# Performance work log

Hardware: AMD Instinct MI355X
Metric: run time of the kernel (lower is better)

## Reference

```python
import jax, jax.numpy as jnp
import numpy as np

L, N, E, H = 1024, 8, 512, 8


def setup_inputs() -> dict:
    key = jax.random.key(0)
    k1, k2, k3, k4 = jax.random.split(key, 4)
    query = jax.random.normal(k1, (L, N, E), dtype=jnp.float32)
    time = jax.random.normal(k2, (L, N, 1), dtype=jnp.float32) * 1000.0  # timestamps
    in_proj_weight = jax.random.normal(k3, (3 * E, E), dtype=jnp.float32) * 0.02
    in_proj_bias = jnp.zeros((3 * E,), dtype=jnp.float32)
    out_proj_weight = jax.random.normal(k4, (E, E), dtype=jnp.float32) * 0.02
    out_proj_bias = jnp.zeros((E,), dtype=jnp.float32)
    return {
        "query": query,
        "time": time,
        "in_proj_weight": in_proj_weight,
        "in_proj_bias": in_proj_bias,
        "out_proj_weight": out_proj_weight,
        "out_proj_bias": out_proj_bias,
    }


def _temporal_mha(query, time, in_proj_weight, in_proj_bias, out_proj_weight, out_proj_bias):
    # Self-attention path of temporal_multi_head_attention_forward (query is key is value).
    tgt_len, bsz, embed_dim = query.shape
    num_heads = H
    head_dim = embed_dim // num_heads
    scaling = float(head_dim) ** -0.5

    # Temporal bias: tt = time.permute(1,0,2) -> (N, L, 1); alpha[b,i,j] = exp((t_bi - t_bj)/1e6)
    tt = jnp.transpose(time, (1, 0, 2))  # (N, L, 1)
    alpha_time = jnp.exp((tt - jnp.reshape(tt, (bsz, 1, tgt_len))) / 1.0e6)  # (N, L, L)

    # Fused in-projection then chunk into q, k, v.
    qkv = query @ in_proj_weight.T + in_proj_bias  # (L, N, 3E)
    q, k, v = jnp.split(qkv, 3, axis=-1)
    q = q * scaling

    def heads(x):  # (L, N, E) -> (N, H, L, hd)
        return jnp.transpose(x.reshape(tgt_len, bsz, num_heads, head_dim), (1, 2, 0, 3))

    q, k, v = heads(q), heads(k), heads(v)

    # Scores with temporal bias injected (broadcast over heads) -- this is the
    # materialized (N, H, L, L) tensor that breaks the SDPA fusion path.
    scores = jnp.einsum("bhld,bhsd->bhls", q, k) * alpha_time[:, None, :, :]
    attn = jax.nn.softmax(scores, axis=-1)  # dropout_p = 0.0 (inference/reference)

    out = jnp.einsum("bhls,bhsd->bhld", attn, v)  # (N, H, L, hd)
    out = jnp.transpose(out, (2, 0, 1, 3)).reshape(tgt_len, bsz, embed_dim)  # (L, N, E)
    return out @ out_proj_weight.T + out_proj_bias


def reference(query, time, in_proj_weight, in_proj_bias, out_proj_weight, out_proj_bias):
    return _temporal_mha(query, time, in_proj_weight, in_proj_bias, out_proj_weight, out_proj_bias)
```

## Files before the change

kernel.cpp:

```cpp
#include <hip/hip_runtime.h>
#include <cstdint>
#include <cstddef>

typedef unsigned short u16;
typedef unsigned int u32;
typedef __attribute__((ext_vector_type(8))) short short8;
typedef __attribute__((ext_vector_type(4))) float f32x4;
typedef __attribute__((ext_vector_type(16))) float f32x16;

#define L_SEQ 1024
#define N_B   8
#define E_DIM 512
#define H_H   8
#define D_H   64
#define M_ROWS 8192

#if __has_builtin(__builtin_amdgcn_exp2f)
#define EXP2(x) __builtin_amdgcn_exp2f(x)
#else
#define EXP2(x) exp2f(x)
#endif

__device__ __forceinline__ u16 f2bf(float f) {
    u32 u = __float_as_uint(f);
    u32 r = (u + 0x7fffu + ((u >> 16) & 1u)) >> 16;
    return (u16)r;
}

__device__ __forceinline__ u32 cvtpk(float lo, float hi_) {
    u32 r;
    asm("v_cvt_pk_bf16_f32 %0, %1, %2" : "=v"(r) : "v"(lo), "v"(hi_));
    return r;
}

__device__ __forceinline__ void gload16(const void* g, void* l) {
    __builtin_amdgcn_global_load_lds(
        (__attribute__((address_space(1))) void*)(g),
        (__attribute__((address_space(3))) void*)(l), 16, 0, 0);
}

__device__ __forceinline__ short8 ldsw(const u16* base, int row, int c) {
    return *reinterpret_cast<const short8*>(
        reinterpret_cast<const char*>(base) + row * 128 + ((c ^ (row & 7)) << 4));
}

__global__ __launch_bounds__(256) void convert_kernel(
    const float* __restrict__ a, const float* __restrict__ b, const float* __restrict__ c,
    u16* __restrict__ ab, u16* __restrict__ bb, u16* __restrict__ cb)
{
    const int NA = M_ROWS * E_DIM / 4;
    const int NB = 1536 * E_DIM / 4;
    const int i4 = blockIdx.x * 256 + threadIdx.x;
    const float* src; u16* dst; int j;
    if (i4 < NA)           { src = a; dst = ab; j = i4; }
    else if (i4 < NA + NB) { src = b; dst = bb; j = i4 - NA; }
    else                   { src = c; dst = cb; j = i4 - NA - NB; }
    const float4 v = reinterpret_cast<const float4*>(src)[j];
    ushort4 o;
    o.x = f2bf(v.x); o.y = f2bf(v.y); o.z = f2bf(v.z); o.w = f2bf(v.w);
    reinterpret_cast<ushort4*>(dst)[j] = o;
}

template <int MODE, int MI>
__global__ __launch_bounds__(256, 2) void gemm_kernel(
    const u16* __restrict__ A, const u16* __restrict__ B,
    const float* __restrict__ bias, const float* __restrict__ tptr,
    u16* __restrict__ qh, u16* __restrict__ kh, u16* __restrict__ vh,
    float* __restrict__ outf)
{
    constexpr int BM = MI * 32;
    __shared__ __align__(16) u16 Asm_[BM * 64];
    __shared__ __align__(16) u16 Bsm[128 * 64];
    const int tid = threadIdx.x;
    const int lane = tid & 63, w = tid >> 6;
    const int wm = w >> 1, wn = w & 1;
    const int m0 = blockIdx.x * BM, n0 = blockIdx.y * 128;

    f32x4 acc[MI][4];
    #pragma unroll
    for (int mi = 0; mi < MI; ++mi)
        #pragma unroll
        for (int ni = 0; ni < 4; ++ni)
            #pragma unroll
            for (int r = 0; r < 4; ++r) acc[mi][ni][r] = 0.f;

    const int srow = (w << 3) + (lane >> 3);
    const int csrc = ((lane & 7) ^ (lane >> 3)) << 3;

    for (int kt = 0; kt < 8; ++kt) {
        __syncthreads();
        #pragma unroll
        for (int i = 0; i < MI; ++i) {
            const int row = (i << 5) + srow;
            gload16(A + (size_t)(m0 + row) * 512 + (kt << 6) + csrc,
                    (char*)Asm_ + (i << 12) + (w << 10));
        }
        #pragma unroll
        for (int i = 0; i < 4; ++i) {
            const int row = (i << 5) + srow;
            gload16(B + (size_t)(n0 + row) * 512 + (kt << 6) + csrc,
                    (char*)Bsm + (i << 12) + (w << 10));
        }
        __syncthreads();
        #pragma unroll
        for (int k01 = 0; k01 < 2; ++k01) {
            short8 af[MI], bfr[4];
            #pragma unroll
            for (int x = 0; x < MI; ++x)
                af[x] = ldsw(Asm_, wm * (MI * 16) + (x << 4) + (lane & 15),
                             (k01 << 2) + (lane >> 4));
            #pragma unroll
            for (int x = 0; x < 4; ++x)
                bfr[x] = ldsw(Bsm, (wn << 6) + (x << 4) + (lane & 15),
                              (k01 << 2) + (lane >> 4));
            __builtin_amdgcn_s_setprio(1);
            #pragma unroll
            for (int mi = 0; mi < MI; ++mi)
                #pragma unroll
                for (int ni = 0; ni < 4; ++ni)
                    acc[mi][ni] = __builtin_amdgcn_mfma_f32_16x16x32_bf16(
                        af[mi], bfr[ni], acc[mi][ni], 0, 0, 0);
            __builtin_amdgcn_s_setprio(0);
        }
    }

    const int nb = n0 + (wn << 6) + (lane & 15);
    const int mb = m0 + wm * (MI * 16) + ((lane >> 4) << 2);
    float bsv[4];
    #pragma unroll
    for (int ni = 0; ni < 4; ++ni) bsv[ni] = bias[nb + (ni << 4)];
    const int sec = n0 >> 9;

    #pragma unroll
    for (int mi = 0; mi < MI; ++mi) {
        #pragma unroll
        for (int r = 0; r < 4; ++r) {
            const int m = mb + (mi << 4) + r;
            float scale = 1.f;
            if (MODE == 0) {
                if (sec == 0)      scale = 0.18033688f * __expf(tptr[m] * 1e-6f);
                else if (sec == 1) scale = __expf(tptr[m] * -1e-6f);
            }
            #pragma unroll
            for (int ni = 0; ni < 4; ++ni) {
                const int n = nb + (ni << 4);
                const float v = acc[mi][ni][r] + bsv[ni];
                if (MODE == 0) {
                    const int l_seq = m >> 3, bb2 = m & 7;
                    const int hh = (n & 511) >> 6, dd = n & 63;
                    u16* dst = (sec == 0) ? qh : (sec == 1) ? kh : vh;
                    dst[(((size_t)(bb2 << 3) + hh) * L_SEQ + l_seq) * D_H + dd] = f2bf(v * scale);
                } else {
                    outf[(size_t)m * 512 + n] = v;
                }
            }
        }
    }
}

__global__ __launch_bounds__(256) void transpose_v(
    const u16* __restrict__ vh, u16* __restrict__ vt)
{
    __shared__ __align__(16) u16 T[64 * 64];
    const int bh = blockIdx.x, kt = blockIdx.y;
    const u16* src = vh + ((size_t)bh * L_SEQ + kt * 64) * D_H;

    #pragma unroll
    for (int rnd = 0; rnd < 2; ++rnd) {
        const int slot = rnd * 256 + threadIdx.x;
        const int row = slot >> 3, c = slot & 7;
        const uint4 v = *reinterpret_cast<const uint4*>(src + row * 64 + c * 8);
        const int cs = c ^ (row & 7) ^ ((row >> 3) & 7);
        *reinterpret_cast<uint4*>(&T[row * 64 + cs * 8]) = v;
    }
    __syncthreads();
    #pragma unroll
    for (int rnd = 0; rnd < 2; ++rnd) {
        const int slot = rnd * 256 + threadIdx.x;
        const int d = slot >> 3, kc = slot & 7;
        u16 tmp[8];
        #pragma unroll
        for (int j = 0; j < 8; ++j) {
            const int row = kc * 8 + j;
            const int col = (((d >> 3) ^ (row & 7) ^ ((row >> 3) & 7)) << 3) + (d & 7);
            tmp[j] = T[row * 64 + col];
        }
        *reinterpret_cast<uint4*>(vt + ((size_t)bh * D_H + d) * L_SEQ + kt * 64 + kc * 8) =
            *reinterpret_cast<uint4*>(tmp);
    }
}

__global__ __launch_bounds__(128) void attn_kernel(
    const u16* __restrict__ qh, const u16* __restrict__ kh,
    const u16* __restrict__ vt, u16* __restrict__ ao)
{
    __shared__ __align__(16) u16 SM[16384];

    const int tid = threadIdx.x;
    const int lane = tid & 63, w = tid >> 6;
    const int hi = lane >> 5, q31 = lane & 31;
    const int bh = blockIdx.x, qt = blockIdx.y;
    const int b = bh >> 3, h = bh & 7;

    const u16* qrow = qh + ((size_t)bh * L_SEQ + qt * 64 + w * 32 + q31) * D_H;
    short8 qf[4];
    #pragma unroll
    for (int ks = 0; ks < 4; ++ks)
        qf[ks] = *reinterpret_cast<const short8*>(qrow + ks * 16 + hi * 8);

    f32x16 oacc[2];
    #pragma unroll
    for (int d = 0; d < 2; ++d)
        #pragma unroll
        for (int r = 0; r < 16; ++r) oacc[d][r] = 0.f;
    float m_run = -1e30f, l_run = 0.f;

    const u16* kbase = kh + (size_t)bh * L_SEQ * D_H;
    const u16* vbase = vt + (size_t)bh * D_H * L_SEQ;
    const int r8 = lane >> 3;
    const int csrc = ((lane & 7) ^ r8) << 3;

    auto stage = [&](int buf, int kt) {
        #pragma unroll
        for (int i = 0; i < 4; ++i) {
            const int row = (w << 5) + (i << 3) + r8;
            gload16(kbase + (size_t)(kt * 64 + row) * 64 + csrc,
                    (char*)SM + buf * 8192 + (w << 12) + (i << 10));
            gload16(vbase + (size_t)row * 1024 + kt * 64 + csrc,
                    (char*)SM + 16384 + buf * 8192 + (w << 12) + (i << 10));
        }
    };

    int cur = 0;
    stage(0, 0);
    __syncthreads();

    for (int kt = 0; kt < 16; ++kt) {
        if (kt < 15) stage(cur ^ 1, kt + 1);
        const u16* Kc = SM + cur * 4096;
        const u16* Vc = SM + 8192 + cur * 4096;

        f32x16 s[2];
        #pragma unroll
        for (int d = 0; d < 2; ++d)
            #pragma unroll
            for (int r = 0; r < 16; ++r) s[d][r] = 0.f;
        __builtin_amdgcn_s_setprio(1);
        #pragma unroll
        for (int ks = 0; ks < 4; ++ks) {
            const int c = 2 * ks + hi;
            const short8 ka0 = ldsw(Kc, q31, c);
            const short8 ka1 = ldsw(Kc, 32 + q31, c);
            s[0] = __builtin_amdgcn_mfma_f32_32x32x16_bf16(ka0, qf[ks], s[0], 0, 0, 0);
            s[1] = __builtin_amdgcn_mfma_f32_32x32x16_bf16(ka1, qf[ks], s[1], 0, 0, 0);
        }
        __builtin_amdgcn_s_setprio(0);

        float pmax = -1e30f;
        #pragma unroll
        for (int hh = 0; hh < 2; ++hh)
            #pragma unroll
            for (int r = 0; r < 16; ++r) pmax = fmaxf(pmax, s[hh][r]);
        pmax = fmaxf(pmax, __shfl_xor(pmax, 32));
        if (!__all(pmax - m_run <= 8.0f)) {
            const float mn = fmaxf(m_run, pmax);
            const float fr = EXP2(m_run - mn);
            l_run *= fr;
            oacc[0] *= fr; oacc[1] *= fr;
            m_run = mn;
        }
        float p[2][16];
        float sum = 0.f;
        #pragma unroll
        for (int hh = 0; hh < 2; ++hh)
            #pragma unroll
            for (int r = 0; r < 16; ++r) {
                const float e = EXP2(s[hh][r] - m_run);
                p[hh][r] = e; sum += e;
            }
        sum += __shfl_xor(sum, 32);
        l_run += sum;

        __builtin_amdgcn_s_setprio(1);
        #pragma unroll
        for (int ks = 0; ks < 4; ++ks) {
            const int e = ks & 1, hh = ks >> 1;
            const u32 pkA = cvtpk(p[hh][8 * e + 0], p[hh][8 * e + 1]);
            const u32 pkB = cvtpk(p[hh][8 * e + 2], p[hh][8 * e + 3]);
            const u32 pkC = cvtpk(p[hh][8 * e + 4], p[hh][8 * e + 5]);
            const u32 pkD = cvtpk(p[hh][8 * e + 6], p[hh][8 * e + 7]);
            const u32 keep0 = hi ? pkC : pkA, keep1 = hi ? pkD : pkB;
            const u32 send0 = hi ? pkA : pkC, send1 = hi ? pkB : pkD;
            const u32 r0 = (u32)__shfl_xor((int)send0, 32);
            const u32 r1 = (u32)__shfl_xor((int)send1, 32);
            union { u32 u[4]; short8 v; } pf;
            pf.u[0] = hi ? r0 : keep0;  pf.u[1] = hi ? r1 : keep1;
            pf.u[2] = hi ? keep0 : r0;  pf.u[3] = hi ? keep1 : r1;
            const int c = 2 * ks + hi;
            const short8 va0 = ldsw(Vc, q31, c);
            const short8 va1 = ldsw(Vc, 32 + q31, c);
            oacc[0] = __builtin_amdgcn_mfma_f32_32x32x16_bf16(va0, pf.v, oacc[0], 0, 0, 0);
            oacc[1] = __builtin_amdgcn_mfma_f32_32x32x16_bf16(va1, pf.v, oacc[1], 0, 0, 0);
        }
        __builtin_amdgcn_s_setprio(0);
        __syncthreads();
        cur ^= 1;
    }

    const float inv = 1.f / l_run;
    float* myO = (float*)SM + w * 2080;
    #pragma unroll
    for (int dh = 0; dh < 2; ++dh)
        #pragma unroll
        for (int r = 0; r < 16; ++r) {
            const int d = dh * 32 + (r & 3) + 8 * (r >> 2) + 4 * hi;
            myO[q31 * 65 + d] = oacc[dh][r] * inv;
        }
    __syncthreads();
    #pragma unroll
    for (int i = 0; i < 4; ++i) {
        const int slot = i * 64 + lane;
        const int qq = slot >> 3, dc = slot & 7;
        u16 outv[8];
        #pragma unroll
        for (int j = 0; j < 8; ++j) outv[j] = f2bf(myO[qq * 65 + dc * 8 + j]);
        const int lrow = qt * 64 + w * 32 + qq;
        *reinterpret_cast<uint4*>(ao + ((size_t)lrow * N_B + b) * E_DIM + h * 64 + dc * 8) =
            *reinterpret_cast<uint4*>(outv);
    }
}

extern "C" void kernel_launch(void* const* d_in, const int* in_sizes, int n_in,
                              void* d_out, int out_size, void* d_ws, size_t ws_size,
                              hipStream_t stream) {
    const float* query = (const float*)d_in[0];
    const float* timep = (const float*)d_in[1];
    const float* w_in  = (const float*)d_in[2];
    const float* b_in  = (const float*)d_in[3];
    const float* w_out = (const float*)d_in[4];
    const float* b_out = (const float*)d_in[5];
    float* out = (float*)d_out;

    u16* ws = (u16*)d_ws;
    const size_t SZ = (size_t)M_ROWS * E_DIM;
    u16* Abf  = ws;
    u16* Wibf = Abf + SZ;
    u16* Wobf = Wibf + 1536 * 512;
    u16* qhb  = Wobf + 512 * 512;
    u16* khb  = qhb + SZ;
    u16* vhb  = khb + SZ;
    u16* vtb  = vhb + SZ;
    u16* aob  = vtb + SZ;

    convert_kernel<<<5120, 256, 0, stream>>>(query, w_in, w_out, Abf, Wibf, Wobf);
    gemm_kernel<0, 4><<<dim3(64, 12), 256, 0, stream>>>(
        Abf, Wibf, b_in, timep, qhb, khb, vhb, nullptr);
    transpose_v<<<dim3(64, 16), 256, 0, stream>>>(vhb, vtb);
    attn_kernel<<<dim3(64, 16), 128, 0, stream>>>(qhb, khb, vtb, aob);
    gemm_kernel<1, 2><<<dim3(128, 4), 256, 0, stream>>>(
        aob, Wobf, b_out, nullptr, nullptr, nullptr, nullptr, out);
}
```

Baseline: 142.7 us.

## Load K/V fragments directly from global into registers in single-wave attention blocks

The attention kernel drops the LDS double-buffered K/V staging and block-level barriers. Each 64-thread block (one wave, 32 query rows) now reads its MFMA operand fragments for K and V straight from global memory into registers. The grid is flattened to 2048 blocks with a swizzled block-to-(head, q-tile) mapping so that blocks sharing a head are likely to hit the same cache. This removes LDS traffic and syncs, but each wave now fetches K/V on its own with no explicit prefetch, which doubles global/L2 reads and exposes load latency.

```diff
diff --git a/kernel.cpp b/kernel.cpp
--- a/kernel.cpp
+++ b/kernel.cpp
@@ -190,19 +190,20 @@
     }
 }
 
-__global__ __launch_bounds__(128) void attn_kernel(
+__global__ __launch_bounds__(64) void attn_kernel(
     const u16* __restrict__ qh, const u16* __restrict__ kh,
     const u16* __restrict__ vt, u16* __restrict__ ao)
 {
-    __shared__ __align__(16) u16 SM[16384];
-
-    const int tid = threadIdx.x;
-    const int lane = tid & 63, w = tid >> 6;
+    __shared__ __align__(16) float myO[32 * 65];
+
+    const int lane = threadIdx.x;
     const int hi = lane >> 5, q31 = lane & 31;
-    const int bh = blockIdx.x, qt = blockIdx.y;
+    const int orig = blockIdx.x;
+    const int swz = (orig & 7) * 256 + (orig >> 3);
+    const int bh = swz >> 5, qt = swz & 31;
     const int b = bh >> 3, h = bh & 7;
 
-    const u16* qrow = qh + ((size_t)bh * L_SEQ + qt * 64 + w * 32 + q31) * D_H;
+    const u16* qrow = qh + ((size_t)bh * L_SEQ + qt * 32 + q31) * D_H;
     short8 qf[4];
     #pragma unroll
     for (int ks = 0; ks < 4; ++ks)
@@ -217,28 +218,21 @@
 
     const u16* kbase = kh + (size_t)bh * L_SEQ * D_H;
     const u16* vbase = vt + (size_t)bh * D_H * L_SEQ;
-    const int r8 = lane >> 3;
-    const int csrc = ((lane & 7) ^ r8) << 3;
-
-    auto stage = [&](int buf, int kt) {
-        #pragma unroll
-        for (int i = 0; i < 4; ++i) {
-            const int row = (w << 5) + (i << 3) + r8;
-            gload16(kbase + (size_t)(kt * 64 + row) * 64 + csrc,
-                    (char*)SM + buf * 8192 + (w << 12) + (i << 10));
-            gload16(vbase + (size_t)row * 1024 + kt * 64 + csrc,
-                    (char*)SM + 16384 + buf * 8192 + (w << 12) + (i << 10));
-        }
-    };
-
-    int cur = 0;
-    stage(0, 0);
-    __syncthreads();
 
     for (int kt = 0; kt < 16; ++kt) {
-        if (kt < 15) stage(cur ^ 1, kt + 1);
-        const u16* Kc = SM + cur * 4096;
-        const u16* Vc = SM + 8192 + cur * 4096;
+        short8 kf0[4], kf1[4], vf0[4], vf1[4];
+        const u16* kp = kbase + (size_t)(kt * 64 + q31) * 64 + hi * 8;
+        #pragma unroll
+        for (int ks = 0; ks < 4; ++ks) {
+            kf0[ks] = *reinterpret_cast<const short8*>(kp + ks * 16);
+            kf1[ks] = *reinterpret_cast<const short8*>(kp + 32 * 64 + ks * 16);
+        }
+        const u16* vp = vbase + (size_t)q31 * 1024 + kt * 64 + hi * 8;
+        #pragma unroll
+        for (int ks = 0; ks < 4; ++ks) {
+            vf0[ks] = *reinterpret_cast<const short8*>(vp + ks * 16);
+            vf1[ks] = *reinterpret_cast<const short8*>(vp + 32 * 1024 + ks * 16);
+        }
 
         f32x16 s[2];
         #pragma unroll
@@ -248,11 +242,8 @@
         __builtin_amdgcn_s_setprio(1);
         #pragma unroll
         for (int ks = 0; ks < 4; ++ks) {
-            const int c = 2 * ks + hi;
-            const short8 ka0 = ldsw(Kc, q31, c);
-            const short8 ka1 = ldsw(Kc, 32 + q31, c);
-            s[0] = __builtin_amdgcn_mfma_f32_32x32x16_bf16(ka0, qf[ks], s[0], 0, 0, 0);
-            s[1] = __builtin_amdgcn_mfma_f32_32x32x16_bf16(ka1, qf[ks], s[1], 0, 0, 0);
+            s[0] = __builtin_amdgcn_mfma_f32_32x32x16_bf16(kf0[ks], qf[ks], s[0], 0, 0, 0);
+            s[1] = __builtin_amdgcn_mfma_f32_32x32x16_bf16(kf1[ks], qf[ks], s[1], 0, 0, 0);
         }
         __builtin_amdgcn_s_setprio(0);
 
@@ -296,19 +287,13 @@
             union { u32 u[4]; short8 v; } pf;
             pf.u[0] = hi ? r0 : keep0;  pf.u[1] = hi ? r1 : keep1;
             pf.u[2] = hi ? keep0 : r0;  pf.u[3] = hi ? keep1 : r1;
-            const int c = 2 * ks + hi;
-            const short8 va0 = ldsw(Vc, q31, c);
-            const short8 va1 = ldsw(Vc, 32 + q31, c);
-            oacc[0] = __builtin_amdgcn_mfma_f32_32x32x16_bf16(va0, pf.v, oacc[0], 0, 0, 0);
-            oacc[1] = __builtin_amdgcn_mfma_f32_32x32x16_bf16(va1, pf.v, oacc[1], 0, 0, 0);
+            oacc[0] = __builtin_amdgcn_mfma_f32_32x32x16_bf16(vf0[ks], pf.v, oacc[0], 0, 0, 0);
+            oacc[1] = __builtin_amdgcn_mfma_f32_32x32x16_bf16(vf1[ks], pf.v, oacc[1], 0, 0, 0);
         }
         __builtin_amdgcn_s_setprio(0);
-        __syncthreads();
-        cur ^= 1;
     }
 
     const float inv = 1.f / l_run;
-    float* myO = (float*)SM + w * 2080;
     #pragma unroll
     for (int dh = 0; dh < 2; ++dh)
         #pragma unroll
@@ -316,7 +301,6 @@
             const int d = dh * 32 + (r & 3) + 8 * (r >> 2) + 4 * hi;
             myO[q31 * 65 + d] = oacc[dh][r] * inv;
         }
-    __syncthreads();
     #pragma unroll
     for (int i = 0; i < 4; ++i) {
         const int slot = i * 64 + lane;
@@ -324,7 +308,7 @@
         u16 outv[8];
         #pragma unroll
         for (int j = 0; j < 8; ++j) outv[j] = f2bf(myO[qq * 65 + dc * 8 + j]);
-        const int lrow = qt * 64 + w * 32 + qq;
+        const int lrow = qt * 32 + qq;
         *reinterpret_cast<uint4*>(ao + ((size_t)lrow * N_B + b) * E_DIM + h * 64 + dc * 8) =
             *reinterpret_cast<uint4*>(outv);
     }
@@ -356,7 +340,7 @@
     gemm_kernel<0, 4><<<dim3(64, 12), 256, 0, stream>>>(
         Abf, Wibf, b_in, timep, qhb, khb, vhb, nullptr);
     transpose_v<<<dim3(64, 16), 256, 0, stream>>>(vhb, vtb);
-    attn_kernel<<<dim3(64, 16), 128, 0, stream>>>(qhb, khb, vtb, aob);
+    attn_kernel<<<2048, 64, 0, stream>>>(qhb, khb, vtb, aob);
     gemm_kernel<1, 2><<<dim3(128, 4), 256, 0, stream>>>(
         aob, Wobf, b_out, nullptr, nullptr, nullptr, nullptr, out);
 }
```

Measured after the change: 172.5 us. 1.21x slower.
